# Performance work log

Hardware: AMD Instinct MI355X
Metric: run time of the kernel (lower is better)

Reference implementation:

```python
import jax, jax.numpy as jnp
import numpy as np

N_QUBITS = 14
STATE_DIM = 2 ** N_QUBITS  # 16384
BATCH, SEQ = 4, 2048


def setup_inputs() -> dict:
    key = jax.random.key(0)
    ks = jax.random.split(key, 5)
    x = jax.random.normal(ks[0], (BATCH, SEQ), dtype=jnp.float32)
    rotation_params = jax.random.normal(ks[1], (N_QUBITS, 3), dtype=jnp.float32)
    entangling_params = jax.random.normal(ks[2], (N_QUBITS - 1,), dtype=jnp.float32)
    # classical_encoder: Linear(1, n_qubits) -> Tanh -> Linear(n_qubits, state_dim) -> Softmax
    W1 = jax.random.normal(ks[3], (1, N_QUBITS), dtype=jnp.float32)
    b1 = jnp.zeros((N_QUBITS,), dtype=jnp.float32)
    W2 = jax.random.normal(ks[4], (N_QUBITS, STATE_DIM), dtype=jnp.float32) * 0.1
    b2 = jnp.zeros((STATE_DIM,), dtype=jnp.float32)
    return {"x": x, "rotation_params": rotation_params,
            "entangling_params": entangling_params,
            "W1": W1, "b1": b1, "W2": W2, "b2": b2}


def reference(x, rotation_params, entangling_params, W1, b1, W2, b2):
    # classical_encoder applied to each scalar x[i,j] -> softmax weights [B,S,D]
    h = jnp.tanh(x[..., None] * W1[0] + b1)          # [B,S,nq]
    w = jax.nn.softmax(h @ W2 + b2, axis=-1)         # [B,S,D]
    # Per-qubit rotation scalar factors (independent of x), multiplied together
    half = rotation_params * 0.5
    c, s = jnp.cos(half), jnp.sin(half)              # [nq,3]
    rot_factors = c[:, 0] * c[:, 1] * c[:, 2] + 1j * (s[:, 0] * s[:, 1] * s[:, 2])
    # Per-pair parameterized-CNOT scalar factors
    cs = jax.nn.sigmoid(entangling_params)
    ent_factors = cs + 1j * (1.0 - cs)
    total = (jnp.prod(rot_factors) * jnp.prod(ent_factors)).astype(jnp.complex64)
    # state starts as e0; all scalar multiplies keep only component 0 nonzero,
    # then elementwise multiply by classical weights.
    out = jnp.zeros(w.shape, dtype=jnp.complex64)
    out = out.at[..., 0].set(total * w[..., 0].astype(jnp.complex64))
    return out
```

## Files before the change

kernel.cpp:

```cpp
#include <hip/hip_runtime.h>
#include <math.h>

constexpr int NQ    = 14;
constexpr int DIM   = 16384;
constexpr int BATCH = 4;
constexpr int SEQ   = 2048;
constexpr int NPOS  = BATCH * SEQ;
constexpr int P     = 4;
constexpr int TPB   = 256;

__device__ __forceinline__ float uniform_f(float v) {
    return __int_as_float(__builtin_amdgcn_readfirstlane(__float_as_int(v)));
}


template <bool CPLX>
__global__ void __launch_bounds__(TPB)
qenc_kernel(const float* __restrict__ x,
            const float* __restrict__ rot,
            const float* __restrict__ ent,
            const float* __restrict__ W1,
            const float* __restrict__ b1,
            const float* __restrict__ W2,
            const float* __restrict__ b2,
            float* __restrict__ out)
{
    __shared__ float sh_h[P * NQ];
    __shared__ float sh_tot_re, sh_tot_im;
    __shared__ float sh_z0[P];
    __shared__ float red[4][P];

    const int tid  = threadIdx.x;
    const int wid  = tid >> 6;
    const int lane = tid & 63;
    const long long pos0 = (long long)blockIdx.x * P;

    if (tid < P * NQ) {
        const int p = tid / NQ;
        const int k = tid - p * NQ;
        sh_h[tid] = tanhf(x[pos0 + p] * W1[k] + b1[k]);
    }
    if (tid == 64) {
        float tre = 1.0f, tim = 0.0f;
        for (int q = 0; q < NQ; ++q) {
            const float a0 = 0.5f * rot[q * 3 + 0];
            const float a1 = 0.5f * rot[q * 3 + 1];
            const float a2 = 0.5f * rot[q * 3 + 2];
            const float fre = cosf(a0) * cosf(a1) * cosf(a2);
            const float fim = sinf(a0) * sinf(a1) * sinf(a2);
            const float nre = tre * fre - tim * fim;
            const float nim = tre * fim + tim * fre;
            tre = nre; tim = nim;
        }
        for (int q = 0; q < NQ - 1; ++q) {
            const float cs  = 1.0f / (1.0f + __expf(-ent[q]));
            const float nre = tre * cs - tim * (1.0f - cs);
            const float nim = tre * (1.0f - cs) + tim * cs;
            tre = nre; tim = nim;
        }
        sh_tot_re = tre; sh_tot_im = tim;
    }
    __syncthreads();

    float h[P][NQ];
#pragma unroll
    for (int p = 0; p < P; ++p)
#pragma unroll
        for (int k = 0; k < NQ; ++k)
            h[p][k] = uniform_f(sh_h[p * NQ + k]);

    float acc[P];
#pragma unroll
    for (int p = 0; p < P; ++p) acc[p] = 0.0f;

    constexpr int ITERS = DIM / (4 * TPB);
    for (int i = 0; i < ITERS; ++i) {
        const int d = 4 * (tid + TPB * i);
        float4 wv[NQ];
#pragma unroll
        for (int k = 0; k < NQ; ++k)
            wv[k] = *reinterpret_cast<const float4*>(W2 + (size_t)k * DIM + d);
        const float4 bb = *reinterpret_cast<const float4*>(b2 + d);
#pragma unroll
        for (int p = 0; p < P; ++p) {
            float za = bb.x, zb = bb.y, zc = bb.z, zd = bb.w;
#pragma unroll
            for (int k = 0; k < NQ; ++k) {
                za = fmaf(h[p][k], wv[k].x, za);
                zb = fmaf(h[p][k], wv[k].y, zb);
                zc = fmaf(h[p][k], wv[k].z, zc);
                zd = fmaf(h[p][k], wv[k].w, zd);
            }
            acc[p] += (__expf(za) + __expf(zb)) + (__expf(zc) + __expf(zd));

            if (d == 0) sh_z0[p] = za;
        }
    }

#pragma unroll
    for (int p = 0; p < P; ++p) {
        float v = acc[p];
#pragma unroll
        for (int off = 32; off > 0; off >>= 1)
            v += __shfl_down(v, off, 64);
        if (lane == 0) red[wid][p] = v;
    }
    __syncthreads();
    if (tid < P) {
        const float denom = (red[0][tid] + red[1][tid]) + (red[2][tid] + red[3][tid]);
        const float w0 = __expf(sh_z0[tid]) / denom;
        const size_t stride = CPLX ? 2 * (size_t)DIM : (size_t)DIM;
        float* rowp = out + (size_t)(pos0 + tid) * stride;
        rowp[0] = sh_tot_re * w0;
        if constexpr (CPLX) rowp[1] = sh_tot_im * w0;
    }
}

extern "C" void kernel_launch(void* const* d_in, const int* in_sizes, int n_in,
                              void* d_out, int out_size, void* d_ws, size_t ws_size,
                              hipStream_t stream) {
    (void)in_sizes; (void)n_in; (void)d_ws; (void)ws_size;
    const float* x   = (const float*)d_in[0];
    const float* rot = (const float*)d_in[1];
    const float* ent = (const float*)d_in[2];
    const float* W1  = (const float*)d_in[3];
    const float* b1  = (const float*)d_in[4];
    const float* W2  = (const float*)d_in[5];
    const float* b2  = (const float*)d_in[6];
    float* out = (float*)d_out;

    hipMemsetAsync(d_out, 0, (size_t)out_size * sizeof(float), stream);

    const long long cplx_elems = (long long)NPOS * 2LL * DIM;
    if ((long long)out_size >= cplx_elems) {
        qenc_kernel<true><<<NPOS / P, TPB, 0, stream>>>(x, rot, ent, W1, b1, W2, b2, out);
    } else {
        qenc_kernel<false><<<NPOS / P, TPB, 0, stream>>>(x, rot, ent, W1, b1, W2, b2, out);
    }
}
```

Baseline: 610.3 us.

## Fuse output zeroing into kernel via interleaved zero-fill blocks with nontemporal stores

Drops the separate hipMemsetAsync and launches twice as many blocks: even blocks zero four output rows with nontemporal vector stores, skipping the element(s) that the odd blocks write, and odd blocks do the softmax-denominator compute as before. This removes a separate memset pass and lets the write-bound zero-fill overlap with the compute-bound work in one launch. The risk is that zero-fill blocks and compute blocks compete for CUs, and that the pos0 indexing must line up with the rows the zero blocks skip.

```diff
diff --git a/kernel.cpp b/kernel.cpp
--- a/kernel.cpp
+++ b/kernel.cpp
@@ -8,6 +8,9 @@
 constexpr int NPOS  = BATCH * SEQ;
 constexpr int P     = 4;
 constexpr int TPB   = 256;
+
+typedef float vf4 __attribute__((ext_vector_type(4)));
+typedef float vf2 __attribute__((ext_vector_type(2)));
 
 __device__ __forceinline__ float uniform_f(float v) {
     return __int_as_float(__builtin_amdgcn_readfirstlane(__float_as_int(v)));
@@ -25,15 +28,51 @@
             const float* __restrict__ b2,
             float* __restrict__ out)
 {
+    const int tid = threadIdx.x;
+
+    if ((blockIdx.x & 1) == 0) {
+        const long long row0 = (long long)(blockIdx.x >> 1) * 4;
+        if constexpr (CPLX) {
+            float* base = out + row0 * (2 * (size_t)DIM);
+#pragma unroll 4
+            for (int i = 0; i < 128; ++i) {
+                const int idx4 = tid + TPB * i;
+                float* p = base + 4 * (size_t)idx4;
+                if ((idx4 & 8191) != 0) {
+                    vf4 z4 = {0.f, 0.f, 0.f, 0.f};
+                    __builtin_nontemporal_store(z4, reinterpret_cast<vf4*>(p));
+                } else {
+                    vf2 z2 = {0.f, 0.f};
+                    __builtin_nontemporal_store(z2, reinterpret_cast<vf2*>(p + 2));
+                }
+            }
+        } else {
+            float* base = out + row0 * (size_t)DIM;
+#pragma unroll 4
+            for (int i = 0; i < 64; ++i) {
+                const int idx4 = tid + TPB * i;
+                float* p = base + 4 * (size_t)idx4;
+                if ((idx4 & 4095) != 0) {
+                    vf4 z4 = {0.f, 0.f, 0.f, 0.f};
+                    __builtin_nontemporal_store(z4, reinterpret_cast<vf4*>(p));
+                } else {
+                    __builtin_nontemporal_store(0.f, p + 1);
+                    vf2 z2 = {0.f, 0.f};
+                    __builtin_nontemporal_store(z2, reinterpret_cast<vf2*>(p + 2));
+                }
+            }
+        }
+        return;
+    }
+
     __shared__ float sh_h[P * NQ];
     __shared__ float sh_tot_re, sh_tot_im;
     __shared__ float sh_z0[P];
     __shared__ float red[4][P];
 
-    const int tid  = threadIdx.x;
     const int wid  = tid >> 6;
     const int lane = tid & 63;
-    const long long pos0 = (long long)blockIdx.x * P;
+    const long long pos0 = (long long)(blockIdx.x >> 1) * P;
 
     if (tid < P * NQ) {
         const int p = tid / NQ;
@@ -92,7 +131,6 @@
                 zd = fmaf(h[p][k], wv[k].w, zd);
             }
             acc[p] += (__expf(za) + __expf(zb)) + (__expf(zc) + __expf(zd));
-
             if (d == 0) sh_z0[p] = za;
         }
     }
@@ -129,12 +167,10 @@
     const float* b2  = (const float*)d_in[6];
     float* out = (float*)d_out;
 
-    hipMemsetAsync(d_out, 0, (size_t)out_size * sizeof(float), stream);
-
     const long long cplx_elems = (long long)NPOS * 2LL * DIM;
     if ((long long)out_size >= cplx_elems) {
-        qenc_kernel<true><<<NPOS / P, TPB, 0, stream>>>(x, rot, ent, W1, b1, W2, b2, out);
+        qenc_kernel<true><<<2 * (NPOS / 4), TPB, 0, stream>>>(x, rot, ent, W1, b1, W2, b2, out);
     } else {
-        qenc_kernel<false><<<NPOS / P, TPB, 0, stream>>>(x, rot, ent, W1, b1, W2, b2, out);
+        qenc_kernel<false><<<2 * (NPOS / 4), TPB, 0, stream>>>(x, rot, ent, W1, b1, W2, b2, out);
     }
 }
```

After: 643.0 us. +5.4%, slower.
